# Optimization experiments

Measured on AMD Instinct MI355X. Metric: run time of the kernel, lower is better.

Reference implementation:

```python
import jax, jax.numpy as jnp
import numpy as np

N_NODES = 500_000
N_EDGES = 16_000_000


def setup_inputs() -> dict:
    key = jax.random.key(0)
    ks = jax.random.split(key, 8)
    x = jax.random.normal(ks[0], (N_NODES, 6), dtype=jnp.float32)
    edge_index = jax.random.randint(ks[1], (2, N_EDGES), 0, N_NODES, dtype=jnp.int64)
    conv_w = jax.random.normal(ks[2], (4, 6), dtype=jnp.float32) * 0.4
    conv_b = jax.random.normal(ks[3], (4,), dtype=jnp.float32) * 0.1
    fc1_w = jax.random.normal(ks[4], (64, 4), dtype=jnp.float32) * 0.5
    fc1_b = jax.random.normal(ks[5], (64,), dtype=jnp.float32) * 0.1
    fc3_w = jax.random.normal(ks[6], (10, 64), dtype=jnp.float32) * 0.125
    fc3_b = jax.random.normal(ks[7], (10,), dtype=jnp.float32) * 0.1
    return {"x": x, "edge_index": edge_index, "conv_w": conv_w, "conv_b": conv_b,
            "fc1_w": fc1_w, "fc1_b": fc1_b, "fc3_w": fc3_w, "fc3_b": fc3_b}


def reference(x, edge_index, conv_w, conv_b, fc1_w, fc1_b, fc3_w, fc3_b):
    n = x.shape[0]
    loop = jnp.arange(n, dtype=edge_index.dtype)
    # PyG GCNConv default: add self-loops, symmetric normalization
    row = jnp.concatenate([edge_index[0], loop])  # source
    col = jnp.concatenate([edge_index[1], loop])  # target (aggregation index)
    deg = jax.ops.segment_sum(jnp.ones_like(col, dtype=x.dtype), col, num_segments=n)
    dinv = jnp.where(deg > 0, deg ** -0.5, 0.0).astype(x.dtype)
    norm = dinv[row] * dinv[col]                  # [E+N]
    h = x @ conv_w.T                              # [N, 4]
    msg = h[row] * norm[:, None]                  # gather + scale
    agg = jax.ops.segment_sum(msg, col, num_segments=n) + conv_b  # scatter-add
    t = jnp.tanh(agg)
    # F.dropout treated as identity (deterministic eval reference)
    g = jnp.mean(t, axis=0, keepdims=True)        # global_mean_pool, batch=None -> [1, 4]
    hdn = jax.nn.relu(g @ fc1_w.T + fc1_b)
    out = hdn @ fc3_w.T + fc3_b                   # [1, output_size]
    return out
```

## Files before the change

kernel.cpp:

```cpp
#include <hip/hip_runtime.h>
#include <hip/hip_fp16.h>
#include <math.h>


constexpr int NP = 1024;
constexpr int SHIFT = 10;
constexpr unsigned MASK = 1023;
constexpr int NPART_MAX = 512;
constexpr int EPB = 8192;
constexpr int BINB = 512;
constexpr int BT = 512;

struct alignas(8) Half4 { __half2 a, b; };


__global__ __launch_bounds__(BINB) void k_bin(const int* __restrict__ row,
                                              const int* __restrict__ col, int E,
                                              int P, int cap, int* __restrict__ cursor,
                                              unsigned* __restrict__ binned) {
    __shared__ unsigned lbuf[EPB];
    __shared__ int lcount[NPART_MAX];
    __shared__ int lbase[NPART_MAX];
    __shared__ int gbase[NPART_MAX];
    __shared__ int lpos[NPART_MAX];
    __shared__ int sc[NPART_MAX];

    int t = threadIdx.x;
    int start = blockIdx.x * EPB;
    int end = min(start + EPB, E);
    bool full = (end - start) == EPB;

    lcount[t] = 0; lpos[t] = 0;
    __syncthreads();

    if (full) {
        const int4* c4 = (const int4*)(col + start);
#pragma unroll
        for (int i = 0; i < EPB / 4 / BINB; ++i) {
            int4 c = c4[t + i * BINB];
            atomicAdd(&lcount[c.x >> SHIFT], 1);
            atomicAdd(&lcount[c.y >> SHIFT], 1);
            atomicAdd(&lcount[c.z >> SHIFT], 1);
            atomicAdd(&lcount[c.w >> SHIFT], 1);
        }
    } else {
        for (int e = start + t; e < end; e += BINB)
            atomicAdd(&lcount[col[e] >> SHIFT], 1);
    }
    __syncthreads();

    sc[t] = lcount[t];
    __syncthreads();
    for (int off = 1; off < NPART_MAX; off <<= 1) {
        int v = (t >= off) ? sc[t - off] : 0;
        __syncthreads();
        sc[t] += v;
        __syncthreads();
    }
    lbase[t] = sc[t] - lcount[t];
    if (t < P) {
        int c = lcount[t];
        gbase[t] = (c > 0) ? atomicAdd(&cursor[t], c) : 0;
    }
    __syncthreads();

    if (full) {
        const int4* c4 = (const int4*)(col + start);
        const int4* r4 = (const int4*)(row + start);
#pragma unroll
        for (int i = 0; i < EPB / 4 / BINB; ++i) {
            int4 c = c4[t + i * BINB];
            int4 r = r4[t + i * BINB];
            int part, slot;
            part = c.x >> SHIFT; slot = atomicAdd(&lpos[part], 1);
            lbuf[lbase[part] + slot] = ((unsigned)r.x << SHIFT) | ((unsigned)c.x & MASK);
            part = c.y >> SHIFT; slot = atomicAdd(&lpos[part], 1);
            lbuf[lbase[part] + slot] = ((unsigned)r.y << SHIFT) | ((unsigned)c.y & MASK);
            part = c.z >> SHIFT; slot = atomicAdd(&lpos[part], 1);
            lbuf[lbase[part] + slot] = ((unsigned)r.z << SHIFT) | ((unsigned)c.z & MASK);
            part = c.w >> SHIFT; slot = atomicAdd(&lpos[part], 1);
            lbuf[lbase[part] + slot] = ((unsigned)r.w << SHIFT) | ((unsigned)c.w & MASK);
        }
    } else {
        for (int e = start + t; e < end; e += BINB) {
            int r = row[e], c = col[e];
            int part = c >> SHIFT;
            int slot = atomicAdd(&lpos[part], 1);
            lbuf[lbase[part] + slot] = ((unsigned)r << SHIFT) | ((unsigned)c & MASK);
        }
    }
    __syncthreads();

    int lane = t & 63;
    int wave = t >> 6;
    const int nwaves = BINB / 64;
    for (int part = wave; part < P; part += nwaves) {
        int cnt = lcount[part];
        if (cnt == 0) continue;
        int lb = lbase[part];
        int gb = gbase[part];
        unsigned* dst = binned + (size_t)part * cap;
        for (int j = lane; j < cnt; j += 64) {
            int slot = gb + j;
            if (slot < cap) dst[slot] = lbuf[lb + j];
        }
    }
}

__global__ __launch_bounds__(BT) void k_part_node(const unsigned* __restrict__ binned,
                                                  const int* __restrict__ cursor, int cap,
                                                  const float* __restrict__ x,
                                                  const float* __restrict__ conv_w, int n,
                                                  Half4* __restrict__ ph,
                                                  float* __restrict__ dinvg) {
    __shared__ int degs[NP];
    __shared__ float w[24];
    int part = blockIdx.x;
    int tid = threadIdx.x;
    if (tid < 24) w[tid] = conv_w[tid];
    for (int i = tid; i < NP; i += BT) degs[i] = 0;
    __syncthreads();
    int cnt = min(cursor[part], cap);
    const unsigned* bin = binned + (size_t)part * cap;
    const uint4* bin4 = (const uint4*)bin;
    int cnt4 = cnt >> 2;
    for (int i = tid; i < cnt4; i += BT) {
        uint4 v = bin4[i];
        atomicAdd(&degs[v.x & MASK], 1);
        atomicAdd(&degs[v.y & MASK], 1);
        atomicAdd(&degs[v.z & MASK], 1);
        atomicAdd(&degs[v.w & MASK], 1);
    }
    for (int e = (cnt4 << 2) + tid; e < cnt; e += BT)
        atomicAdd(&degs[bin[e] & MASK], 1);
    __syncthreads();
    int base = part * NP;
    for (int i = tid; i < NP; i += BT) {
        int node = base + i;
        if (node >= n) continue;
        float dinv = rsqrtf((float)(degs[i] + 1));
        const float* xr = x + (size_t)node * 6;
        float2 a = *(const float2*)xr;
        float2 b = *(const float2*)(xr + 2);
        float2 cc = *(const float2*)(xr + 4);
        float xv[6] = {a.x, a.y, b.x, b.y, cc.x, cc.y};
        float h0 = 0.f, h1 = 0.f, h2 = 0.f, h3 = 0.f;
#pragma unroll
        for (int j = 0; j < 6; ++j) {
            h0 += xv[j] * w[j];
            h1 += xv[j] * w[6 + j];
            h2 += xv[j] * w[12 + j];
            h3 += xv[j] * w[18 + j];
        }
        Half4 o;
        o.a = __floats2half2_rn(h0 * dinv, h1 * dinv);
        o.b = __floats2half2_rn(h2 * dinv, h3 * dinv);
        ph[node] = o;
        dinvg[node] = dinv;
    }
}

__device__ __forceinline__ void acc_edge(float* __restrict__ S, unsigned v,
                                         const Half4& h) {
    float2 a = __half22float2(h.a), b = __half22float2(h.b);
    float* s = &S[(v & MASK) * 5];
    unsafeAtomicAdd(s + 0, a.x);
    unsafeAtomicAdd(s + 1, a.y);
    unsafeAtomicAdd(s + 2, b.x);
    unsafeAtomicAdd(s + 3, b.y);
}

__global__ __launch_bounds__(BT) void k_acc2(const unsigned* __restrict__ binned,
                                             const int* __restrict__ cursor, int cap,
                                             const Half4* __restrict__ ph, int SUB,
                                             float4* __restrict__ Spart) {
    __shared__ float S[NP * 5];
    int part = blockIdx.x / SUB;
    int sub = blockIdx.x - part * SUB;
    int tid = threadIdx.x;
    for (int i = tid; i < NP * 5; i += BT) S[i] = 0.f;
    __syncthreads();
    int cnt = min(cursor[part], cap);
    const unsigned* bin = binned + (size_t)part * cap;
    const uint4* bin4 = (const uint4*)bin;
    int cnt4 = cnt >> 2;
    int chunk4 = (cnt4 + SUB - 1) / SUB;
    int s4 = sub * chunk4;
    int e4 = min(cnt4, s4 + chunk4);

    int i = s4 + tid;
    for (; i + BT < e4; i += 2 * BT) {
        uint4 v0 = bin4[i];
        uint4 v1 = bin4[i + BT];
        Half4 h0 = ph[v0.x >> SHIFT];
        Half4 h1 = ph[v0.y >> SHIFT];
        Half4 h2 = ph[v0.z >> SHIFT];
        Half4 h3 = ph[v0.w >> SHIFT];
        Half4 h4 = ph[v1.x >> SHIFT];
        Half4 h5 = ph[v1.y >> SHIFT];
        Half4 h6 = ph[v1.z >> SHIFT];
        Half4 h7 = ph[v1.w >> SHIFT];
        acc_edge(S, v0.x, h0); acc_edge(S, v0.y, h1);
        acc_edge(S, v0.z, h2); acc_edge(S, v0.w, h3);
        acc_edge(S, v1.x, h4); acc_edge(S, v1.y, h5);
        acc_edge(S, v1.z, h6); acc_edge(S, v1.w, h7);
    }
    for (; i < e4; i += BT) {
        uint4 v = bin4[i];
        Half4 h0 = ph[v.x >> SHIFT];
        Half4 h1 = ph[v.y >> SHIFT];
        Half4 h2 = ph[v.z >> SHIFT];
        Half4 h3 = ph[v.w >> SHIFT];
        acc_edge(S, v.x, h0); acc_edge(S, v.y, h1);
        acc_edge(S, v.z, h2); acc_edge(S, v.w, h3);
    }
    if (sub == SUB - 1) {
        for (int e = (cnt4 << 2) + tid; e < cnt; e += BT)
            acc_edge(S, bin[e], ph[bin[e] >> SHIFT]);
    }
    __syncthreads();
    float4* dst = Spart + (size_t)blockIdx.x * NP;
    for (int k = tid; k < NP; k += BT) {
        float4 o;
        o.x = S[k * 5 + 0]; o.y = S[k * 5 + 1];
        o.z = S[k * 5 + 2]; o.w = S[k * 5 + 3];
        dst[k] = o;
    }
}

__global__ __launch_bounds__(BT) void k_tanh(const float4* __restrict__ Spart,
                                             const Half4* __restrict__ ph,
                                             const float* __restrict__ dinvg,
                                             const float* __restrict__ conv_b,
                                             int n, int SUB, float* __restrict__ gsum) {
    int node = blockIdx.x * BT + threadIdx.x;
    float4 acc = {0.f, 0.f, 0.f, 0.f};
    if (node < n) {
        int part = node >> SHIFT;
        int local = node & MASK;
        float4 s = {0.f, 0.f, 0.f, 0.f};
        for (int sub = 0; sub < SUB; ++sub) {
            float4 t = Spart[((size_t)(part * SUB + sub)) * NP + local];
            s.x += t.x; s.y += t.y; s.z += t.z; s.w += t.w;
        }
        float di = dinvg[node];
        Half4 hp = ph[node];
        float2 pa = __half22float2(hp.a), pb = __half22float2(hp.b);
        acc.x = tanhf(di * (s.x + pa.x) + conv_b[0]);
        acc.y = tanhf(di * (s.y + pa.y) + conv_b[1]);
        acc.z = tanhf(di * (s.z + pb.x) + conv_b[2]);
        acc.w = tanhf(di * (s.w + pb.y) + conv_b[3]);
    }
#pragma unroll
    for (int off = 32; off > 0; off >>= 1) {
        acc.x += __shfl_down(acc.x, off);
        acc.y += __shfl_down(acc.y, off);
        acc.z += __shfl_down(acc.z, off);
        acc.w += __shfl_down(acc.w, off);
    }
    __shared__ float4 red[BT / 64];
    int lane = threadIdx.x & 63, wv = threadIdx.x >> 6;
    if (lane == 0) red[wv] = acc;
    __syncthreads();
    if (threadIdx.x == 0) {
        float4 tt = red[0];
        for (int k = 1; k < BT / 64; ++k) {
            tt.x += red[k].x; tt.y += red[k].y; tt.z += red[k].z; tt.w += red[k].w;
        }
        unsafeAtomicAdd(&gsum[0], tt.x);
        unsafeAtomicAdd(&gsum[1], tt.y);
        unsafeAtomicAdd(&gsum[2], tt.z);
        unsafeAtomicAdd(&gsum[3], tt.w);
    }
}

__global__ void k_head(const float* __restrict__ gsum,
                       const float* __restrict__ fc1w, const float* __restrict__ fc1b,
                       const float* __restrict__ fc3w, const float* __restrict__ fc3b,
                       float* __restrict__ out, int n) {
    __shared__ float hdn[64];
    int t = threadIdx.x;
    float g[4];
    float inv_n = 1.0f / (float)n;
#pragma unroll
    for (int j = 0; j < 4; ++j) g[j] = gsum[j] * inv_n;
    if (t < 64) {
        float a = fc1b[t];
#pragma unroll
        for (int j = 0; j < 4; ++j) a += g[j] * fc1w[t * 4 + j];
        hdn[t] = fmaxf(a, 0.f);
    }
    __syncthreads();
    if (t < 10) {
        float a = fc3b[t];
#pragma unroll
        for (int k = 0; k < 64; ++k) a += hdn[k] * fc3w[t * 64 + k];
        out[t] = a;
    }
}


__global__ void k_deg(const int* __restrict__ col, int n_edges, int* __restrict__ deg) {
    int t = blockIdx.x * blockDim.x + threadIdx.x;
    int base = t * 4;
    if (base + 4 <= n_edges) {
        int4 c = *(const int4*)(col + base);
        atomicAdd(&deg[c.x], 1); atomicAdd(&deg[c.y], 1);
        atomicAdd(&deg[c.z], 1); atomicAdd(&deg[c.w], 1);
    } else {
        for (int e = base; e < n_edges; ++e) atomicAdd(&deg[col[e]], 1);
    }
}

__global__ void k_node(const float* __restrict__ x, const float* __restrict__ conv_w,
                       const int* __restrict__ deg, float4* __restrict__ p, int n) {
    int i = blockIdx.x * blockDim.x + threadIdx.x;
    if (i >= n) return;
    const float* xr = x + (size_t)i * 6;
    float2 a = *(const float2*)xr;
    float2 b = *(const float2*)(xr + 2);
    float2 c = *(const float2*)(xr + 4);
    float xv[6] = {a.x, a.y, b.x, b.y, c.x, c.y};
    float dinv = rsqrtf((float)(deg[i] + 1));
    float h0 = 0.f, h1 = 0.f, h2 = 0.f, h3 = 0.f;
#pragma unroll
    for (int j = 0; j < 6; ++j) {
        h0 += xv[j] * conv_w[j];
        h1 += xv[j] * conv_w[6 + j];
        h2 += xv[j] * conv_w[12 + j];
        h3 += xv[j] * conv_w[18 + j];
    }
    float4 o; o.x = h0 * dinv; o.y = h1 * dinv; o.z = h2 * dinv; o.w = h3 * dinv;
    p[i] = o;
}

__global__ void k_scatter(const int* __restrict__ row, const int* __restrict__ col, int n_edges,
                          const float4* __restrict__ p, float* __restrict__ S) {
    int t = blockIdx.x * blockDim.x + threadIdx.x;
    int base = t * 2;
    if (base + 2 <= n_edges) {
        int2 r = *(const int2*)(row + base);
        int2 c = *(const int2*)(col + base);
        float4 p0 = p[r.x], p1 = p[r.y];
        float* s0 = S + 4 * c.x;
        unsafeAtomicAdd(s0 + 0, p0.x); unsafeAtomicAdd(s0 + 1, p0.y);
        unsafeAtomicAdd(s0 + 2, p0.z); unsafeAtomicAdd(s0 + 3, p0.w);
        float* s1 = S + 4 * c.y;
        unsafeAtomicAdd(s1 + 0, p1.x); unsafeAtomicAdd(s1 + 1, p1.y);
        unsafeAtomicAdd(s1 + 2, p1.z); unsafeAtomicAdd(s1 + 3, p1.w);
    } else {
        for (int e = base; e < n_edges; ++e) {
            int r = row[e], c = col[e];
            float4 pv = p[r];
            float* s = S + 4 * c;
            unsafeAtomicAdd(s + 0, pv.x); unsafeAtomicAdd(s + 1, pv.y);
            unsafeAtomicAdd(s + 2, pv.z); unsafeAtomicAdd(s + 3, pv.w);
        }
    }
}

__global__ void k_reduce(const float4* __restrict__ S4, const float4* __restrict__ p,
                         const int* __restrict__ deg, const float* __restrict__ conv_b,
                         int n, float* __restrict__ gsum) {
    int i = blockIdx.x * blockDim.x + threadIdx.x;
    float4 v = {0.f, 0.f, 0.f, 0.f};
    if (i < n) {
        float dinv = rsqrtf((float)(deg[i] + 1));
        float4 s = S4[i];
        float4 pp = p[i];
        v.x = tanhf(dinv * (s.x + pp.x) + conv_b[0]);
        v.y = tanhf(dinv * (s.y + pp.y) + conv_b[1]);
        v.z = tanhf(dinv * (s.z + pp.z) + conv_b[2]);
        v.w = tanhf(dinv * (s.w + pp.w) + conv_b[3]);
    }
#pragma unroll
    for (int off = 32; off > 0; off >>= 1) {
        v.x += __shfl_down(v.x, off);
        v.y += __shfl_down(v.y, off);
        v.z += __shfl_down(v.z, off);
        v.w += __shfl_down(v.w, off);
    }
    __shared__ float4 lds[4];
    int lane = threadIdx.x & 63, w = threadIdx.x >> 6;
    if (lane == 0) lds[w] = v;
    __syncthreads();
    if (threadIdx.x == 0) {
        float4 tt = lds[0];
        for (int k = 1; k < 4; ++k) {
            tt.x += lds[k].x; tt.y += lds[k].y; tt.z += lds[k].z; tt.w += lds[k].w;
        }
        unsafeAtomicAdd(&gsum[0], tt.x); unsafeAtomicAdd(&gsum[1], tt.y);
        unsafeAtomicAdd(&gsum[2], tt.z); unsafeAtomicAdd(&gsum[3], tt.w);
    }
}


extern "C" void kernel_launch(void* const* d_in, const int* in_sizes, int n_in,
                              void* d_out, int out_size, void* d_ws, size_t ws_size,
                              hipStream_t stream) {
    const float* x      = (const float*)d_in[0];
    const int*   ei     = (const int*)d_in[1];
    const float* conv_w = (const float*)d_in[2];
    const float* conv_b = (const float*)d_in[3];
    const float* fc1w   = (const float*)d_in[4];
    const float* fc1b   = (const float*)d_in[5];
    const float* fc3w   = (const float*)d_in[6];
    const float* fc3b   = (const float*)d_in[7];

    int n = in_sizes[0] / 6;
    int E = in_sizes[1] / 2;
    const int* row = ei;
    const int* col = ei + E;

    int P = (n + NP - 1) / NP;
    int avg = (E + P - 1) / P;
    int cap = ((avg + avg / 32 + 256) + 15) & ~15;

    size_t off = 0;
    size_t cursor_off = off;          off += (size_t)P * sizeof(int);
    off = (off + 15) & ~(size_t)15;
    size_t gsum_off = off;            off += 4 * sizeof(float);
    size_t zero_end = off;
    off = (off + 15) & ~(size_t)15;
    size_t dinv_off = off;            off += (size_t)n * sizeof(float);
    off = (off + 15) & ~(size_t)15;
    size_t ph_off = off;              off += (size_t)n * sizeof(Half4);
    off = (off + 15) & ~(size_t)15;
    size_t bin_off = off;             off += (size_t)P * cap * sizeof(unsigned);
    off = (off + 255) & ~(size_t)255;
    size_t spart_off = off;
    size_t spart_bytes1 = (size_t)P * NP * sizeof(float4);

    char* ws = (char*)d_ws;
    int SUB = 0;
    if (ws_size >= spart_off + 2 * spart_bytes1 && P <= NPART_MAX && n < (1 << 22)) SUB = 2;
    else if (ws_size >= spart_off + spart_bytes1 && P <= NPART_MAX && n < (1 << 22)) SUB = 1;

    if (SUB > 0) {
        int* cursor = (int*)(ws + cursor_off);
        float* gsum = (float*)(ws + gsum_off);
        float* dinvg = (float*)(ws + dinv_off);
        Half4* ph = (Half4*)(ws + ph_off);
        unsigned* binned = (unsigned*)(ws + bin_off);
        float4* Spart = (float4*)(ws + spart_off);

        hipMemsetAsync(d_ws, 0, zero_end, stream);
        int bin_blocks = (E + EPB - 1) / EPB;
        k_bin<<<bin_blocks, BINB, 0, stream>>>(row, col, E, P, cap, cursor, binned);
        k_part_node<<<P, BT, 0, stream>>>(binned, cursor, cap, x, conv_w, n, ph, dinvg);
        k_acc2<<<P * SUB, BT, 0, stream>>>(binned, cursor, cap, ph, SUB, Spart);
        k_tanh<<<(n + BT - 1) / BT, BT, 0, stream>>>(Spart, ph, dinvg, conv_b, n, SUB, gsum);
        k_head<<<1, 64, 0, stream>>>(gsum, fc1w, fc1b, fc3w, fc3b, (float*)d_out, n);
    } else {
        size_t o = 0;
        int* deg = (int*)(ws + o);      o += (size_t)n * sizeof(int);
        o = (o + 15) & ~(size_t)15;
        float* S = (float*)(ws + o);    o += (size_t)n * 4 * sizeof(float);
        float* gsum = (float*)(ws + o);
        size_t zend = o + 4 * sizeof(float);
        o = (zend + 15) & ~(size_t)15;
        float4* p = (float4*)(ws + o);

        hipMemsetAsync(d_ws, 0, zend, stream);
        int t1 = (E + 3) / 4;
        k_deg<<<(t1 + 255) / 256, 256, 0, stream>>>(col, E, deg);
        k_node<<<(n + 255) / 256, 256, 0, stream>>>(x, conv_w, deg, p, n);
        int t3 = (E + 1) / 2;
        k_scatter<<<(t3 + 255) / 256, 256, 0, stream>>>(row, col, E, p, S);
        k_reduce<<<(n + 255) / 256, 256, 0, stream>>>((const float4*)S, p, deg, conv_b, n, gsum);
        k_head<<<1, 64, 0, stream>>>(gsum, fc1w, fc1b, fc3w, fc3b, (float*)d_out, n);
    }
}
```

Before: 679.8 us.

## Replace random gather with two-phase source/target binning and FP8 value propagation

The new default path bins edges twice. A first pass bins by target with 16-bit local ids and only computes degrees. A second pass bins by source, so each source block can read its contiguous slice of node features into shared memory, convert them to FP8, and redistribute the values to target partitions. The accumulate kernel then reads packed values and column ids with no random global gather. The aim is to turn the scattered reads of ph into sequential traffic, at the cost of several extra passes over the edge list, more workspace, and reduced precision from FP8 messages.

```diff
diff --git a/kernel.cpp b/kernel.cpp
--- a/kernel.cpp
+++ b/kernel.cpp
@@ -10,15 +10,19 @@
 constexpr int EPB = 8192;
 constexpr int BINB = 512;
 constexpr int BT = 512;
+constexpr int SUBD = 4;
+constexpr int SUBA = 4;
+constexpr int SUBV = 4;
+constexpr int CHMAX = 8704;
 
 struct alignas(8) Half4 { __half2 a, b; };
-
-
-__global__ __launch_bounds__(BINB) void k_bin(const int* __restrict__ row,
-                                              const int* __restrict__ col, int E,
-                                              int P, int cap, int* __restrict__ cursor,
-                                              unsigned* __restrict__ binned) {
-    __shared__ unsigned lbuf[EPB];
+typedef float floatx2 __attribute__((ext_vector_type(2)));
+
+
+__global__ __launch_bounds__(BINB) void k_binT2(const int* __restrict__ col, int E,
+                                                int P, int cap, int* __restrict__ cursorT,
+                                                unsigned short* __restrict__ binT) {
+    __shared__ unsigned short lbuf[EPB];
     __shared__ int lcount[NPART_MAX];
     __shared__ int lbase[NPART_MAX];
     __shared__ int gbase[NPART_MAX];
@@ -60,33 +64,31 @@
     lbase[t] = sc[t] - lcount[t];
     if (t < P) {
         int c = lcount[t];
-        gbase[t] = (c > 0) ? atomicAdd(&cursor[t], c) : 0;
+        gbase[t] = (c > 0) ? atomicAdd(&cursorT[t], c) : 0;
     }
     __syncthreads();
 
     if (full) {
         const int4* c4 = (const int4*)(col + start);
-        const int4* r4 = (const int4*)(row + start);
 #pragma unroll
         for (int i = 0; i < EPB / 4 / BINB; ++i) {
             int4 c = c4[t + i * BINB];
-            int4 r = r4[t + i * BINB];
             int part, slot;
             part = c.x >> SHIFT; slot = atomicAdd(&lpos[part], 1);
-            lbuf[lbase[part] + slot] = ((unsigned)r.x << SHIFT) | ((unsigned)c.x & MASK);
+            lbuf[lbase[part] + slot] = (unsigned short)(c.x & MASK);
             part = c.y >> SHIFT; slot = atomicAdd(&lpos[part], 1);
-            lbuf[lbase[part] + slot] = ((unsigned)r.y << SHIFT) | ((unsigned)c.y & MASK);
+            lbuf[lbase[part] + slot] = (unsigned short)(c.y & MASK);
             part = c.z >> SHIFT; slot = atomicAdd(&lpos[part], 1);
-            lbuf[lbase[part] + slot] = ((unsigned)r.z << SHIFT) | ((unsigned)c.z & MASK);
+            lbuf[lbase[part] + slot] = (unsigned short)(c.z & MASK);
             part = c.w >> SHIFT; slot = atomicAdd(&lpos[part], 1);
-            lbuf[lbase[part] + slot] = ((unsigned)r.w << SHIFT) | ((unsigned)c.w & MASK);
+            lbuf[lbase[part] + slot] = (unsigned short)(c.w & MASK);
         }
     } else {
         for (int e = start + t; e < end; e += BINB) {
-            int r = row[e], c = col[e];
+            int c = col[e];
             int part = c >> SHIFT;
             int slot = atomicAdd(&lpos[part], 1);
-            lbuf[lbase[part] + slot] = ((unsigned)r << SHIFT) | ((unsigned)c & MASK);
+            lbuf[lbase[part] + slot] = (unsigned short)(c & MASK);
         }
     }
     __syncthreads();
@@ -99,7 +101,7 @@
         if (cnt == 0) continue;
         int lb = lbase[part];
         int gb = gbase[part];
-        unsigned* dst = binned + (size_t)part * cap;
+        unsigned short* dst = binT + (size_t)part * cap;
         for (int j = lane; j < cnt; j += 64) {
             int slot = gb + j;
             if (slot < cap) dst[slot] = lbuf[lb + j];
@@ -107,116 +109,277 @@
     }
 }
 
-__global__ __launch_bounds__(BT) void k_part_node(const unsigned* __restrict__ binned,
-                                                  const int* __restrict__ cursor, int cap,
-                                                  const float* __restrict__ x,
-                                                  const float* __restrict__ conv_w, int n,
-                                                  Half4* __restrict__ ph,
-                                                  float* __restrict__ dinvg) {
+
+__global__ __launch_bounds__(BT) void k_degS(const unsigned short* __restrict__ binT,
+                                             const int* __restrict__ cursorT, int cap,
+                                             int* __restrict__ degpart) {
     __shared__ int degs[NP];
+    int part = blockIdx.x >> 2;
+    int sub = blockIdx.x & 3;
+    int tid = threadIdx.x;
+    for (int i = tid; i < NP; i += BT) degs[i] = 0;
+    __syncthreads();
+    int cnt = min(cursorT[part], cap);
+    int chunk = (cnt + SUBD - 1) / SUBD;
+    int s = sub * chunk;
+    int e = min(cnt, s + chunk);
+    const unsigned short* bin = binT + (size_t)part * cap;
+    for (int i = s + tid; i < e; i += BT)
+        atomicAdd(&degs[bin[i]], 1);
+    __syncthreads();
+    int* dst = degpart + (size_t)blockIdx.x * NP;
+    for (int i = tid; i < NP; i += BT) dst[i] = degs[i];
+}
+
+
+__global__ __launch_bounds__(BT) void k_node2(const int* __restrict__ degpart,
+                                              const float* __restrict__ x,
+                                              const float* __restrict__ conv_w, int n,
+                                              Half4* __restrict__ ph,
+                                              float* __restrict__ dinvg) {
     __shared__ float w[24];
-    int part = blockIdx.x;
     int tid = threadIdx.x;
     if (tid < 24) w[tid] = conv_w[tid];
-    for (int i = tid; i < NP; i += BT) degs[i] = 0;
-    __syncthreads();
-    int cnt = min(cursor[part], cap);
-    const unsigned* bin = binned + (size_t)part * cap;
-    const uint4* bin4 = (const uint4*)bin;
-    int cnt4 = cnt >> 2;
-    for (int i = tid; i < cnt4; i += BT) {
-        uint4 v = bin4[i];
-        atomicAdd(&degs[v.x & MASK], 1);
-        atomicAdd(&degs[v.y & MASK], 1);
-        atomicAdd(&degs[v.z & MASK], 1);
-        atomicAdd(&degs[v.w & MASK], 1);
-    }
-    for (int e = (cnt4 << 2) + tid; e < cnt; e += BT)
-        atomicAdd(&degs[bin[e] & MASK], 1);
-    __syncthreads();
+    __syncthreads();
+    int i = blockIdx.x * BT + tid;
+    if (i >= n) return;
+    int part = i >> SHIFT;
+    int local = i & MASK;
+    const int* dp = degpart + (size_t)part * SUBD * NP + local;
+    int deg = dp[0] + dp[NP] + dp[2 * NP] + dp[3 * NP];
+    float dinv = rsqrtf((float)(deg + 1));
+    const float* xr = x + (size_t)i * 6;
+    float2 a = *(const float2*)xr;
+    float2 b = *(const float2*)(xr + 2);
+    float2 cc = *(const float2*)(xr + 4);
+    float xv[6] = {a.x, a.y, b.x, b.y, cc.x, cc.y};
+    float h0 = 0.f, h1 = 0.f, h2 = 0.f, h3 = 0.f;
+#pragma unroll
+    for (int j = 0; j < 6; ++j) {
+        h0 += xv[j] * w[j];
+        h1 += xv[j] * w[6 + j];
+        h2 += xv[j] * w[12 + j];
+        h3 += xv[j] * w[18 + j];
+    }
+    Half4 o;
+    o.a = __floats2half2_rn(h0 * dinv, h1 * dinv);
+    o.b = __floats2half2_rn(h2 * dinv, h3 * dinv);
+    ph[i] = o;
+    dinvg[i] = dinv;
+}
+
+
+__global__ __launch_bounds__(BINB) void k_binS(const int* __restrict__ row,
+                                               const int* __restrict__ col, int E,
+                                               int P, int cap, int* __restrict__ cursorS,
+                                               unsigned* __restrict__ binS) {
+    __shared__ unsigned lbuf[EPB];
+    __shared__ int lcount[NPART_MAX];
+    __shared__ int lbase[NPART_MAX];
+    __shared__ int gbase[NPART_MAX];
+    __shared__ int lpos[NPART_MAX];
+    __shared__ int sc[NPART_MAX];
+
+    int t = threadIdx.x;
+    int start = blockIdx.x * EPB;
+    int end = min(start + EPB, E);
+    bool full = (end - start) == EPB;
+
+    lcount[t] = 0; lpos[t] = 0;
+    __syncthreads();
+
+    if (full) {
+        const int4* r4 = (const int4*)(row + start);
+#pragma unroll
+        for (int i = 0; i < EPB / 4 / BINB; ++i) {
+            int4 r = r4[t + i * BINB];
+            atomicAdd(&lcount[r.x >> SHIFT], 1);
+            atomicAdd(&lcount[r.y >> SHIFT], 1);
+            atomicAdd(&lcount[r.z >> SHIFT], 1);
+            atomicAdd(&lcount[r.w >> SHIFT], 1);
+        }
+    } else {
+        for (int e = start + t; e < end; e += BINB)
+            atomicAdd(&lcount[row[e] >> SHIFT], 1);
+    }
+    __syncthreads();
+
+    sc[t] = lcount[t];
+    __syncthreads();
+    for (int off = 1; off < NPART_MAX; off <<= 1) {
+        int v = (t >= off) ? sc[t - off] : 0;
+        __syncthreads();
+        sc[t] += v;
+        __syncthreads();
+    }
+    lbase[t] = sc[t] - lcount[t];
+    if (t < P) {
+        int c = lcount[t];
+        gbase[t] = (c > 0) ? atomicAdd(&cursorS[t], c) : 0;
+    }
+    __syncthreads();
+
+    if (full) {
+        const int4* r4 = (const int4*)(row + start);
+        const int4* c4 = (const int4*)(col + start);
+#pragma unroll
+        for (int i = 0; i < EPB / 4 / BINB; ++i) {
+            int4 r = r4[t + i * BINB];
+            int4 c = c4[t + i * BINB];
+            int part, slot;
+            part = r.x >> SHIFT; slot = atomicAdd(&lpos[part], 1);
+            lbuf[lbase[part] + slot] = ((unsigned)c.x << SHIFT) | ((unsigned)r.x & MASK);
+            part = r.y >> SHIFT; slot = atomicAdd(&lpos[part], 1);
+            lbuf[lbase[part] + slot] = ((unsigned)c.y << SHIFT) | ((unsigned)r.y & MASK);
+            part = r.z >> SHIFT; slot = atomicAdd(&lpos[part], 1);
+            lbuf[lbase[part] + slot] = ((unsigned)c.z << SHIFT) | ((unsigned)r.z & MASK);
+            part = r.w >> SHIFT; slot = atomicAdd(&lpos[part], 1);
+            lbuf[lbase[part] + slot] = ((unsigned)c.w << SHIFT) | ((unsigned)r.w & MASK);
+        }
+    } else {
+        for (int e = start + t; e < end; e += BINB) {
+            int r = row[e], c = col[e];
+            int part = r >> SHIFT;
+            int slot = atomicAdd(&lpos[part], 1);
+            lbuf[lbase[part] + slot] = ((unsigned)c << SHIFT) | ((unsigned)r & MASK);
+        }
+    }
+    __syncthreads();
+
+    int lane = t & 63;
+    int wave = t >> 6;
+    const int nwaves = BINB / 64;
+    for (int part = wave; part < P; part += nwaves) {
+        int cnt = lcount[part];
+        if (cnt == 0) continue;
+        int lb = lbase[part];
+        int gb = gbase[part];
+        unsigned* dst = binS + (size_t)part * cap;
+        for (int j = lane; j < cnt; j += 64) {
+            int slot = gb + j;
+            if (slot < cap) dst[slot] = lbuf[lb + j];
+        }
+    }
+}
+
+
+__global__ __launch_bounds__(BINB) void k_attach(const unsigned* __restrict__ binS,
+                                                 const int* __restrict__ cursorS, int cap,
+                                                 const Half4* __restrict__ ph, int n,
+                                                 int P, int* __restrict__ cursorV,
+                                                 unsigned* __restrict__ valV,
+                                                 unsigned short* __restrict__ clV) {
+    __shared__ unsigned pslice[NP];
+    __shared__ unsigned lbufV[CHMAX];
+    __shared__ unsigned short lbufC[CHMAX];
+    __shared__ int lcount[NPART_MAX];
+    __shared__ int lbase[NPART_MAX];
+    __shared__ int gbase[NPART_MAX];
+    __shared__ int lpos[NPART_MAX];
+    __shared__ int sc[NPART_MAX];
+
+    int part = blockIdx.x >> 2;
+    int sub = blockIdx.x & 3;
+    int t = threadIdx.x;
+
     int base = part * NP;
-    for (int i = tid; i < NP; i += BT) {
+    for (int i = t; i < NP; i += BINB) {
         int node = base + i;
-        if (node >= n) continue;
-        float dinv = rsqrtf((float)(degs[i] + 1));
-        const float* xr = x + (size_t)node * 6;
-        float2 a = *(const float2*)xr;
-        float2 b = *(const float2*)(xr + 2);
-        float2 cc = *(const float2*)(xr + 4);
-        float xv[6] = {a.x, a.y, b.x, b.y, cc.x, cc.y};
-        float h0 = 0.f, h1 = 0.f, h2 = 0.f, h3 = 0.f;
-#pragma unroll
-        for (int j = 0; j < 6; ++j) {
-            h0 += xv[j] * w[j];
-            h1 += xv[j] * w[6 + j];
-            h2 += xv[j] * w[12 + j];
-            h3 += xv[j] * w[18 + j];
-        }
-        Half4 o;
-        o.a = __floats2half2_rn(h0 * dinv, h1 * dinv);
-        o.b = __floats2half2_rn(h2 * dinv, h3 * dinv);
-        ph[node] = o;
-        dinvg[node] = dinv;
-    }
-}
-
-__device__ __forceinline__ void acc_edge(float* __restrict__ S, unsigned v,
-                                         const Half4& h) {
-    float2 a = __half22float2(h.a), b = __half22float2(h.b);
-    float* s = &S[(v & MASK) * 5];
-    unsafeAtomicAdd(s + 0, a.x);
-    unsafeAtomicAdd(s + 1, a.y);
-    unsafeAtomicAdd(s + 2, b.x);
-    unsafeAtomicAdd(s + 3, b.y);
-}
-
-__global__ __launch_bounds__(BT) void k_acc2(const unsigned* __restrict__ binned,
-                                             const int* __restrict__ cursor, int cap,
-                                             const Half4* __restrict__ ph, int SUB,
+        unsigned wv = 0;
+        if (node < n) {
+            Half4 hp = ph[node];
+            float2 pa = __half22float2(hp.a);
+            float2 pb = __half22float2(hp.b);
+            int w = __builtin_amdgcn_cvt_pk_fp8_f32(pa.x, pa.y, 0, false);
+            w = __builtin_amdgcn_cvt_pk_fp8_f32(pb.x, pb.y, w, true);
+            wv = (unsigned)w;
+        }
+        pslice[i] = wv;
+    }
+    lcount[t] = 0; lpos[t] = 0;
+    __syncthreads();
+
+    int cnt = min(cursorS[part], cap);
+    int chunk = (cnt + SUBA - 1) / SUBA;
+    int s = sub * chunk;
+    int e = min(cnt, s + chunk);
+    const unsigned* bin = binS + (size_t)part * cap;
+
+    for (int i = s + t; i < e; i += BINB)
+        atomicAdd(&lcount[bin[i] >> 20], 1);
+    __syncthreads();
+
+    sc[t] = lcount[t];
+    __syncthreads();
+    for (int off = 1; off < NPART_MAX; off <<= 1) {
+        int v = (t >= off) ? sc[t - off] : 0;
+        __syncthreads();
+        sc[t] += v;
+        __syncthreads();
+    }
+    lbase[t] = sc[t] - lcount[t];
+    if (t < P) {
+        int c = lcount[t];
+        gbase[t] = (c > 0) ? atomicAdd(&cursorV[t], c) : 0;
+    }
+    __syncthreads();
+
+    for (int i = s + t; i < e; i += BINB) {
+        unsigned rec = bin[i];
+        int tpart = (int)(rec >> 20);
+        int slot = lbase[tpart] + atomicAdd(&lpos[tpart], 1);
+        lbufV[slot] = pslice[rec & MASK];
+        lbufC[slot] = (unsigned short)((rec >> SHIFT) & MASK);
+    }
+    __syncthreads();
+
+    int lane = t & 63;
+    int wave = t >> 6;
+    const int nwaves = BINB / 64;
+    for (int tp = wave; tp < P; tp += nwaves) {
+        int c = lcount[tp];
+        if (c == 0) continue;
+        int lb = lbase[tp];
+        int gb = gbase[tp];
+        unsigned* dv = valV + (size_t)tp * cap;
+        unsigned short* dc = clV + (size_t)tp * cap;
+        for (int j = lane; j < c; j += 64) {
+            int slot = gb + j;
+            if (slot < cap) {
+                dv[slot] = lbufV[lb + j];
+                dc[slot] = lbufC[lb + j];
+            }
+        }
+    }
+}
+
+
+__global__ __launch_bounds__(BT) void k_accV(const unsigned* __restrict__ valV,
+                                             const unsigned short* __restrict__ clV,
+                                             const int* __restrict__ cursorV, int cap,
                                              float4* __restrict__ Spart) {
     __shared__ float S[NP * 5];
-    int part = blockIdx.x / SUB;
-    int sub = blockIdx.x - part * SUB;
+    int part = blockIdx.x >> 2;
+    int sub = blockIdx.x & 3;
     int tid = threadIdx.x;
     for (int i = tid; i < NP * 5; i += BT) S[i] = 0.f;
     __syncthreads();
-    int cnt = min(cursor[part], cap);
-    const unsigned* bin = binned + (size_t)part * cap;
-    const uint4* bin4 = (const uint4*)bin;
-    int cnt4 = cnt >> 2;
-    int chunk4 = (cnt4 + SUB - 1) / SUB;
-    int s4 = sub * chunk4;
-    int e4 = min(cnt4, s4 + chunk4);
-
-    int i = s4 + tid;
-    for (; i + BT < e4; i += 2 * BT) {
-        uint4 v0 = bin4[i];
-        uint4 v1 = bin4[i + BT];
-        Half4 h0 = ph[v0.x >> SHIFT];
-        Half4 h1 = ph[v0.y >> SHIFT];
-        Half4 h2 = ph[v0.z >> SHIFT];
-        Half4 h3 = ph[v0.w >> SHIFT];
-        Half4 h4 = ph[v1.x >> SHIFT];
-        Half4 h5 = ph[v1.y >> SHIFT];
-        Half4 h6 = ph[v1.z >> SHIFT];
-        Half4 h7 = ph[v1.w >> SHIFT];
-        acc_edge(S, v0.x, h0); acc_edge(S, v0.y, h1);
-        acc_edge(S, v0.z, h2); acc_edge(S, v0.w, h3);
-        acc_edge(S, v1.x, h4); acc_edge(S, v1.y, h5);
-        acc_edge(S, v1.z, h6); acc_edge(S, v1.w, h7);
-    }
-    for (; i < e4; i += BT) {
-        uint4 v = bin4[i];
-        Half4 h0 = ph[v.x >> SHIFT];
-        Half4 h1 = ph[v.y >> SHIFT];
-        Half4 h2 = ph[v.z >> SHIFT];
-        Half4 h3 = ph[v.w >> SHIFT];
-        acc_edge(S, v.x, h0); acc_edge(S, v.y, h1);
-        acc_edge(S, v.z, h2); acc_edge(S, v.w, h3);
-    }
-    if (sub == SUB - 1) {
-        for (int e = (cnt4 << 2) + tid; e < cnt; e += BT)
-            acc_edge(S, bin[e], ph[bin[e] >> SHIFT]);
+    int cnt = min(cursorV[part], cap);
+    int chunk = (cnt + SUBV - 1) / SUBV;
+    int s = sub * chunk;
+    int e = min(cnt, s + chunk);
+    const unsigned* vp = valV + (size_t)part * cap;
+    const unsigned short* cp = clV + (size_t)part * cap;
+    for (int i = s + tid; i < e; i += BT) {
+        unsigned val = vp[i];
+        int cl = cp[i];
+        floatx2 lo = __builtin_amdgcn_cvt_pk_f32_fp8((int)val, false);
+        floatx2 hi = __builtin_amdgcn_cvt_pk_f32_fp8((int)val, true);
+        float* sp = &S[cl * 5];
+        unsafeAtomicAdd(sp + 0, lo[0]);
+        unsafeAtomicAdd(sp + 1, lo[1]);
+        unsafeAtomicAdd(sp + 2, hi[0]);
+        unsafeAtomicAdd(sp + 3, hi[1]);
     }
     __syncthreads();
     float4* dst = Spart + (size_t)blockIdx.x * NP;
@@ -227,6 +390,7 @@
         dst[k] = o;
     }
 }
+
 
 __global__ __launch_bounds__(BT) void k_tanh(const float4* __restrict__ Spart,
                                              const Half4* __restrict__ ph,
@@ -300,97 +464,195 @@
 }
 
 
-__global__ void k_deg(const int* __restrict__ col, int n_edges, int* __restrict__ deg) {
-    int t = blockIdx.x * blockDim.x + threadIdx.x;
-    int base = t * 4;
-    if (base + 4 <= n_edges) {
-        int4 c = *(const int4*)(col + base);
-        atomicAdd(&deg[c.x], 1); atomicAdd(&deg[c.y], 1);
-        atomicAdd(&deg[c.z], 1); atomicAdd(&deg[c.w], 1);
+__global__ __launch_bounds__(BINB) void k_bin(const int* __restrict__ row,
+                                              const int* __restrict__ col, int E,
+                                              int P, int cap, int* __restrict__ cursor,
+                                              unsigned* __restrict__ binned) {
+    __shared__ unsigned lbuf[EPB];
+    __shared__ int lcount[NPART_MAX];
+    __shared__ int lbase[NPART_MAX];
+    __shared__ int gbase[NPART_MAX];
+    __shared__ int lpos[NPART_MAX];
+    __shared__ int sc[NPART_MAX];
+
+    int t = threadIdx.x;
+    int start = blockIdx.x * EPB;
+    int end = min(start + EPB, E);
+    bool full = (end - start) == EPB;
+
+    lcount[t] = 0; lpos[t] = 0;
+    __syncthreads();
+    if (full) {
+        const int4* c4 = (const int4*)(col + start);
+#pragma unroll
+        for (int i = 0; i < EPB / 4 / BINB; ++i) {
+            int4 c = c4[t + i * BINB];
+            atomicAdd(&lcount[c.x >> SHIFT], 1);
+            atomicAdd(&lcount[c.y >> SHIFT], 1);
+            atomicAdd(&lcount[c.z >> SHIFT], 1);
+            atomicAdd(&lcount[c.w >> SHIFT], 1);
+        }
     } else {
-        for (int e = base; e < n_edges; ++e) atomicAdd(&deg[col[e]], 1);
-    }
-}
-
-__global__ void k_node(const float* __restrict__ x, const float* __restrict__ conv_w,
-                       const int* __restrict__ deg, float4* __restrict__ p, int n) {
-    int i = blockIdx.x * blockDim.x + threadIdx.x;
-    if (i >= n) return;
-    const float* xr = x + (size_t)i * 6;
-    float2 a = *(const float2*)xr;
-    float2 b = *(const float2*)(xr + 2);
-    float2 c = *(const float2*)(xr + 4);
-    float xv[6] = {a.x, a.y, b.x, b.y, c.x, c.y};
-    float dinv = rsqrtf((float)(deg[i] + 1));
-    float h0 = 0.f, h1 = 0.f, h2 = 0.f, h3 = 0.f;
-#pragma unroll
-    for (int j = 0; j < 6; ++j) {
-        h0 += xv[j] * conv_w[j];
-        h1 += xv[j] * conv_w[6 + j];
-        h2 += xv[j] * conv_w[12 + j];
-        h3 += xv[j] * conv_w[18 + j];
-    }
-    float4 o; o.x = h0 * dinv; o.y = h1 * dinv; o.z = h2 * dinv; o.w = h3 * dinv;
-    p[i] = o;
-}
-
-__global__ void k_scatter(const int* __restrict__ row, const int* __restrict__ col, int n_edges,
-                          const float4* __restrict__ p, float* __restrict__ S) {
-    int t = blockIdx.x * blockDim.x + threadIdx.x;
-    int base = t * 2;
-    if (base + 2 <= n_edges) {
-        int2 r = *(const int2*)(row + base);
-        int2 c = *(const int2*)(col + base);
-        float4 p0 = p[r.x], p1 = p[r.y];
-        float* s0 = S + 4 * c.x;
-        unsafeAtomicAdd(s0 + 0, p0.x); unsafeAtomicAdd(s0 + 1, p0.y);
-        unsafeAtomicAdd(s0 + 2, p0.z); unsafeAtomicAdd(s0 + 3, p0.w);
-        float* s1 = S + 4 * c.y;
-        unsafeAtomicAdd(s1 + 0, p1.x); unsafeAtomicAdd(s1 + 1, p1.y);
-        unsafeAtomicAdd(s1 + 2, p1.z); unsafeAtomicAdd(s1 + 3, p1.w);
+        for (int e = start + t; e < end; e += BINB)
+            atomicAdd(&lcount[col[e] >> SHIFT], 1);
+    }
+    __syncthreads();
+    sc[t] = lcount[t];
+    __syncthreads();
+    for (int off = 1; off < NPART_MAX; off <<= 1) {
+        int v = (t >= off) ? sc[t - off] : 0;
+        __syncthreads();
+        sc[t] += v;
+        __syncthreads();
+    }
+    lbase[t] = sc[t] - lcount[t];
+    if (t < P) {
+        int c = lcount[t];
+        gbase[t] = (c > 0) ? atomicAdd(&cursor[t], c) : 0;
+    }
+    __syncthreads();
+    if (full) {
+        const int4* c4 = (const int4*)(col + start);
+        const int4* r4 = (const int4*)(row + start);
+#pragma unroll
+        for (int i = 0; i < EPB / 4 / BINB; ++i) {
+            int4 c = c4[t + i * BINB];
+            int4 r = r4[t + i * BINB];
+            int part, slot;
+            part = c.x >> SHIFT; slot = atomicAdd(&lpos[part], 1);
+            lbuf[lbase[part] + slot] = ((unsigned)r.x << SHIFT) | ((unsigned)c.x & MASK);
+            part = c.y >> SHIFT; slot = atomicAdd(&lpos[part], 1);
+            lbuf[lbase[part] + slot] = ((unsigned)r.y << SHIFT) | ((unsigned)c.y & MASK);
+            part = c.z >> SHIFT; slot = atomicAdd(&lpos[part], 1);
+            lbuf[lbase[part] + slot] = ((unsigned)r.z << SHIFT) | ((unsigned)c.z & MASK);
+            part = c.w >> SHIFT; slot = atomicAdd(&lpos[part], 1);
+            lbuf[lbase[part] + slot] = ((unsigned)r.w << SHIFT) | ((unsigned)c.w & MASK);
+        }
     } else {
-        for (int e = base; e < n_edges; ++e) {
+        for (int e = start + t; e < end; e += BINB) {
             int r = row[e], c = col[e];
-            float4 pv = p[r];
-            float* s = S + 4 * c;
-            unsafeAtomicAdd(s + 0, pv.x); unsafeAtomicAdd(s + 1, pv.y);
-            unsafeAtomicAdd(s + 2, pv.z); unsafeAtomicAdd(s + 3, pv.w);
-        }
-    }
-}
-
-__global__ void k_reduce(const float4* __restrict__ S4, const float4* __restrict__ p,
-                         const int* __restrict__ deg, const float* __restrict__ conv_b,
-                         int n, float* __restrict__ gsum) {
-    int i = blockIdx.x * blockDim.x + threadIdx.x;
-    float4 v = {0.f, 0.f, 0.f, 0.f};
-    if (i < n) {
-        float dinv = rsqrtf((float)(deg[i] + 1));
-        float4 s = S4[i];
-        float4 pp = p[i];
-        v.x = tanhf(dinv * (s.x + pp.x) + conv_b[0]);
-        v.y = tanhf(dinv * (s.y + pp.y) + conv_b[1]);
-        v.z = tanhf(dinv * (s.z + pp.z) + conv_b[2]);
-        v.w = tanhf(dinv * (s.w + pp.w) + conv_b[3]);
-    }
-#pragma unroll
-    for (int off = 32; off > 0; off >>= 1) {
-        v.x += __shfl_down(v.x, off);
-        v.y += __shfl_down(v.y, off);
-        v.z += __shfl_down(v.z, off);
-        v.w += __shfl_down(v.w, off);
-    }
-    __shared__ float4 lds[4];
-    int lane = threadIdx.x & 63, w = threadIdx.x >> 6;
-    if (lane == 0) lds[w] = v;
-    __syncthreads();
-    if (threadIdx.x == 0) {
-        float4 tt = lds[0];
-        for (int k = 1; k < 4; ++k) {
-            tt.x += lds[k].x; tt.y += lds[k].y; tt.z += lds[k].z; tt.w += lds[k].w;
-        }
-        unsafeAtomicAdd(&gsum[0], tt.x); unsafeAtomicAdd(&gsum[1], tt.y);
-        unsafeAtomicAdd(&gsum[2], tt.z); unsafeAtomicAdd(&gsum[3], tt.w);
+            int part = c >> SHIFT;
+            int slot = atomicAdd(&lpos[part], 1);
+            lbuf[lbase[part] + slot] = ((unsigned)r << SHIFT) | ((unsigned)c & MASK);
+        }
+    }
+    __syncthreads();
+    int lane = t & 63;
+    int wave = t >> 6;
+    const int nwaves = BINB / 64;
+    for (int part = wave; part < P; part += nwaves) {
+        int cnt = lcount[part];
+        if (cnt == 0) continue;
+        int lb = lbase[part];
+        int gb = gbase[part];
+        unsigned* dst = binned + (size_t)part * cap;
+        for (int j = lane; j < cnt; j += 64) {
+            int slot = gb + j;
+            if (slot < cap) dst[slot] = lbuf[lb + j];
+        }
+    }
+}
+
+__global__ __launch_bounds__(BT) void k_part_node(const unsigned* __restrict__ binned,
+                                                  const int* __restrict__ cursor, int cap,
+                                                  const float* __restrict__ x,
+                                                  const float* __restrict__ conv_w, int n,
+                                                  Half4* __restrict__ ph,
+                                                  float* __restrict__ dinvg) {
+    __shared__ int degs[NP];
+    __shared__ float w[24];
+    int part = blockIdx.x;
+    int tid = threadIdx.x;
+    if (tid < 24) w[tid] = conv_w[tid];
+    for (int i = tid; i < NP; i += BT) degs[i] = 0;
+    __syncthreads();
+    int cnt = min(cursor[part], cap);
+    const unsigned* bin = binned + (size_t)part * cap;
+    const uint4* bin4 = (const uint4*)bin;
+    int cnt4 = cnt >> 2;
+    for (int i = tid; i < cnt4; i += BT) {
+        uint4 v = bin4[i];
+        atomicAdd(&degs[v.x & MASK], 1);
+        atomicAdd(&degs[v.y & MASK], 1);
+        atomicAdd(&degs[v.z & MASK], 1);
+        atomicAdd(&degs[v.w & MASK], 1);
+    }
+    for (int e = (cnt4 << 2) + tid; e < cnt; e += BT)
+        atomicAdd(&degs[bin[e] & MASK], 1);
+    __syncthreads();
+    int base = part * NP;
+    for (int i = tid; i < NP; i += BT) {
+        int node = base + i;
+        if (node >= n) continue;
+        float dinv = rsqrtf((float)(degs[i] + 1));
+        const float* xr = x + (size_t)node * 6;
+        float2 a = *(const float2*)xr;
+        float2 b = *(const float2*)(xr + 2);
+        float2 cc = *(const float2*)(xr + 4);
+        float xv[6] = {a.x, a.y, b.x, b.y, cc.x, cc.y};
+        float h0 = 0.f, h1 = 0.f, h2 = 0.f, h3 = 0.f;
+#pragma unroll
+        for (int j = 0; j < 6; ++j) {
+            h0 += xv[j] * w[j];
+            h1 += xv[j] * w[6 + j];
+            h2 += xv[j] * w[12 + j];
+            h3 += xv[j] * w[18 + j];
+        }
+        Half4 o;
+        o.a = __floats2half2_rn(h0 * dinv, h1 * dinv);
+        o.b = __floats2half2_rn(h2 * dinv, h3 * dinv);
+        ph[node] = o;
+        dinvg[node] = dinv;
+    }
+}
+
+__device__ __forceinline__ void acc_edge(float* __restrict__ S, unsigned v,
+                                         const Half4& h) {
+    float2 a = __half22float2(h.a), b = __half22float2(h.b);
+    float* s = &S[(v & MASK) * 5];
+    unsafeAtomicAdd(s + 0, a.x);
+    unsafeAtomicAdd(s + 1, a.y);
+    unsafeAtomicAdd(s + 2, b.x);
+    unsafeAtomicAdd(s + 3, b.y);
+}
+
+__global__ __launch_bounds__(BT) void k_acc2(const unsigned* __restrict__ binned,
+                                             const int* __restrict__ cursor, int cap,
+                                             const Half4* __restrict__ ph, int SUB,
+                                             float4* __restrict__ Spart) {
+    __shared__ float S[NP * 5];
+    int part = blockIdx.x / SUB;
+    int sub = blockIdx.x - part * SUB;
+    int tid = threadIdx.x;
+    for (int i = tid; i < NP * 5; i += BT) S[i] = 0.f;
+    __syncthreads();
+    int cnt = min(cursor[part], cap);
+    const unsigned* bin = binned + (size_t)part * cap;
+    const uint4* bin4 = (const uint4*)bin;
+    int cnt4 = cnt >> 2;
+    int chunk4 = (cnt4 + SUB - 1) / SUB;
+    int s4 = sub * chunk4;
+    int e4 = min(cnt4, s4 + chunk4);
+    for (int i = s4 + tid; i < e4; i += BT) {
+        uint4 v = bin4[i];
+        Half4 h0 = ph[v.x >> SHIFT];
+        Half4 h1 = ph[v.y >> SHIFT];
+        Half4 h2 = ph[v.z >> SHIFT];
+        Half4 h3 = ph[v.w >> SHIFT];
+        acc_edge(S, v.x, h0); acc_edge(S, v.y, h1);
+        acc_edge(S, v.z, h2); acc_edge(S, v.w, h3);
+    }
+    if (sub == SUB - 1) {
+        for (int e = (cnt4 << 2) + tid; e < cnt; e += BT)
+            acc_edge(S, bin[e], ph[bin[e] >> SHIFT]);
+    }
+    __syncthreads();
+    float4* dst = Spart + (size_t)blockIdx.x * NP;
+    for (int k = tid; k < NP; k += BT) {
+        float4 o;
+        o.x = S[k * 5 + 0]; o.y = S[k * 5 + 1];
+        o.z = S[k * 5 + 2]; o.w = S[k * 5 + 3];
+        dst[k] = o;
     }
 }
 
@@ -416,58 +678,93 @@
     int avg = (E + P - 1) / P;
     int cap = ((avg + avg / 32 + 256) + 15) & ~15;
 
+    char* ws = (char*)d_ws;
+    bool ok = (P <= NPART_MAX) && (n < (1 << 22)) && ((cap + SUBA - 1) / SUBA <= CHMAX);
+
     size_t off = 0;
-    size_t cursor_off = off;          off += (size_t)P * sizeof(int);
-    off = (off + 15) & ~(size_t)15;
-    size_t gsum_off = off;            off += 4 * sizeof(float);
+    size_t curT_off = off;   off += (size_t)P * sizeof(int);
+    size_t curS_off = off;   off += (size_t)P * sizeof(int);
+    size_t curV_off = off;   off += (size_t)P * sizeof(int);
+    size_t gsum_off = off;   off += 4 * sizeof(float);
     size_t zero_end = off;
     off = (off + 15) & ~(size_t)15;
-    size_t dinv_off = off;            off += (size_t)n * sizeof(float);
+    size_t dinv_off = off;   off += (size_t)n * sizeof(float);
     off = (off + 15) & ~(size_t)15;
-    size_t ph_off = off;              off += (size_t)n * sizeof(Half4);
+    size_t ph_off = off;     off += (size_t)n * sizeof(Half4);
     off = (off + 15) & ~(size_t)15;
-    size_t bin_off = off;             off += (size_t)P * cap * sizeof(unsigned);
+    size_t degp_off = off;   off += (size_t)P * SUBD * NP * sizeof(int);
+    off = (off + 15) & ~(size_t)15;
+    size_t binT_off = off;   off += (size_t)P * cap * sizeof(unsigned short);
+    off = (off + 15) & ~(size_t)15;
+    size_t binS_off = off;   off += (size_t)P * cap * sizeof(unsigned);
+    off = (off + 15) & ~(size_t)15;
+    size_t valV_off = off;   off += (size_t)P * cap * sizeof(unsigned);
+    off = (off + 15) & ~(size_t)15;
+    size_t clV_off = off;    off += (size_t)P * cap * sizeof(unsigned short);
     off = (off + 255) & ~(size_t)255;
-    size_t spart_off = off;
-    size_t spart_bytes1 = (size_t)P * NP * sizeof(float4);
-
-    char* ws = (char*)d_ws;
-    int SUB = 0;
-    if (ws_size >= spart_off + 2 * spart_bytes1 && P <= NPART_MAX && n < (1 << 22)) SUB = 2;
-    else if (ws_size >= spart_off + spart_bytes1 && P <= NPART_MAX && n < (1 << 22)) SUB = 1;
-
-    if (SUB > 0) {
-        int* cursor = (int*)(ws + cursor_off);
+    size_t spart_off = off;  off += (size_t)P * SUBV * NP * sizeof(float4);
+    size_t need_new = off;
+
+    if (ok && ws_size >= need_new) {
+        int* cursorT = (int*)(ws + curT_off);
+        int* cursorS = (int*)(ws + curS_off);
+        int* cursorV = (int*)(ws + curV_off);
         float* gsum = (float*)(ws + gsum_off);
         float* dinvg = (float*)(ws + dinv_off);
         Half4* ph = (Half4*)(ws + ph_off);
-        unsigned* binned = (unsigned*)(ws + bin_off);
+        int* degpart = (int*)(ws + degp_off);
+        unsigned short* binT = (unsigned short*)(ws + binT_off);
+        unsigned* binS = (unsigned*)(ws + binS_off);
+        unsigned* valV = (unsigned*)(ws + valV_off);
+        unsigned short* clV = (unsigned short*)(ws + clV_off);
         float4* Spart = (float4*)(ws + spart_off);
 
-        hipMemsetAsync(d_ws, 0, zero_end, stream);
+        (void)hipMemsetAsync(d_ws, 0, zero_end, stream);
+        int bin_blocks = (E + EPB - 1) / EPB;
+        k_binT2<<<bin_blocks, BINB, 0, stream>>>(col, E, P, cap, cursorT, binT);
+        k_degS<<<P * SUBD, BT, 0, stream>>>(binT, cursorT, cap, degpart);
+        k_node2<<<(n + BT - 1) / BT, BT, 0, stream>>>(degpart, x, conv_w, n, ph, dinvg);
+        k_binS<<<bin_blocks, BINB, 0, stream>>>(row, col, E, P, cap, cursorS, binS);
+        k_attach<<<P * SUBA, BINB, 0, stream>>>(binS, cursorS, cap, ph, n, P, cursorV, valV, clV);
+        k_accV<<<P * SUBV, BT, 0, stream>>>(valV, clV, cursorV, cap, Spart);
+        k_tanh<<<(n + BT - 1) / BT, BT, 0, stream>>>(Spart, ph, dinvg, conv_b, n, SUBV, gsum);
+        k_head<<<1, 64, 0, stream>>>(gsum, fc1w, fc1b, fc3w, fc3b, (float*)d_out, n);
+        return;
+    }
+
+    size_t o = 0;
+    size_t f_cur = o;        o += (size_t)P * sizeof(int);
+    o = (o + 15) & ~(size_t)15;
+    size_t f_gsum = o;       o += 4 * sizeof(float);
+    size_t f_zero = o + 4 * sizeof(float);
+    o = (f_zero + 15) & ~(size_t)15;
+    size_t f_dinv = o;       o += (size_t)n * sizeof(float);
+    o = (o + 15) & ~(size_t)15;
+    size_t f_ph = o;         o += (size_t)n * sizeof(Half4);
+    o = (o + 15) & ~(size_t)15;
+    size_t f_bin = o;        o += (size_t)P * cap * sizeof(unsigned);
+    o = (o + 255) & ~(size_t)255;
+    size_t f_spart = o;
+    size_t spart1 = (size_t)P * NP * sizeof(float4);
+
+    int SUB = 0;
+    if (ok && ws_size >= f_spart + 2 * spart1) SUB = 2;
+    else if (ok && ws_size >= f_spart + spart1) SUB = 1;
+
+    if (SUB > 0) {
+        int* cursor = (int*)(ws + f_cur);
+        float* gsum = (float*)(ws + f_gsum);
+        float* dinvg = (float*)(ws + f_dinv);
+        Half4* ph = (Half4*)(ws + f_ph);
+        unsigned* binned = (unsigned*)(ws + f_bin);
+        float4* Spart = (float4*)(ws + f_spart);
+
+        (void)hipMemsetAsync(d_ws, 0, f_zero, stream);
         int bin_blocks = (E + EPB - 1) / EPB;
         k_bin<<<bin_blocks, BINB, 0, stream>>>(row, col, E, P, cap, cursor, binned);
         k_part_node<<<P, BT, 0, stream>>>(binned, cursor, cap, x, conv_w, n, ph, dinvg);
         k_acc2<<<P * SUB, BT, 0, stream>>>(binned, cursor, cap, ph, SUB, Spart);
         k_tanh<<<(n + BT - 1) / BT, BT, 0, stream>>>(Spart, ph, dinvg, conv_b, n, SUB, gsum);
         k_head<<<1, 64, 0, stream>>>(gsum, fc1w, fc1b, fc3w, fc3b, (float*)d_out, n);
-    } else {
-        size_t o = 0;
-        int* deg = (int*)(ws + o);      o += (size_t)n * sizeof(int);
-        o = (o + 15) & ~(size_t)15;
-        float* S = (float*)(ws + o);    o += (size_t)n * 4 * sizeof(float);
-        float* gsum = (float*)(ws + o);
-        size_t zend = o + 4 * sizeof(float);
-        o = (zend + 15) & ~(size_t)15;
-        float4* p = (float4*)(ws + o);
-
-        hipMemsetAsync(d_ws, 0, zend, stream);
-        int t1 = (E + 3) / 4;
-        k_deg<<<(t1 + 255) / 256, 256, 0, stream>>>(col, E, deg);
-        k_node<<<(n + 255) / 256, 256, 0, stream>>>(x, conv_w, deg, p, n);
-        int t3 = (E + 1) / 2;
-        k_scatter<<<(t3 + 255) / 256, 256, 0, stream>>>(row, col, E, p, S);
-        k_reduce<<<(n + 255) / 256, 256, 0, stream>>>((const float4*)S, p, deg, conv_b, n, gsum);
-        k_head<<<1, 64, 0, stream>>>(gsum, fc1w, fc1b, fc3w, fc3b, (float*)d_out, n);
-    }
-}
+    }
+}
```

Result: slower. 909.9 us (+33.8%).
